# Kernel tuning notes

Measured on AMD Instinct MI355X. Metric: run time of the kernel, lower is better.

Reference implementation:

```python
import jax, jax.numpy as jnp
import numpy as np

L = 10           # outer iterations (module arg L -> sinkhorn n_iter)
N_INNER = 1      # n_inner_iter=1 in SinkhornLoss.forward
EPS = 1.0        # entropic regularization epsilon


def setup_inputs() -> dict:
    key = jax.random.key(0)
    kx, ky = jax.random.split(key)
    x = jax.random.normal(kx, (8192, 32), dtype=jnp.float32)
    y = jax.random.normal(ky, (8192, 32), dtype=jnp.float32)
    return {"x": x, "y": y}


def _sinkhorn_loss(x, y):
    n, m = x.shape[0], y.shape[0]
    # sqeuclidean cdist: [n, m]
    C = (x * x).sum(1)[:, None] + (y * y).sum(1)[None, :] - 2.0 * (x @ y.T)
    # uniform marginals mu = 1/n, nu = 1/m (mu=None, nu=None in source)
    logmu = -jnp.log(jnp.asarray(n, C.dtype))
    lognu = -jnp.log(jnp.asarray(m, C.dtype))
    f0 = jnp.zeros((n,), C.dtype)
    g0 = jnp.zeros((m,), C.dtype)

    def body(carry, _):
        f, g = carry
        # log-domain Sinkhorn updates (stable logsumexp form)
        f = EPS * (logmu - jax.nn.logsumexp((g[None, :] - C) / EPS, axis=1))
        g = EPS * (lognu - jax.nn.logsumexp((f[:, None] - C) / EPS, axis=0))
        return (f, g), None

    (f, g), _ = jax.lax.scan(body, (f0, g0), None, length=L * N_INNER)
    gamma = jnp.exp((f[:, None] + g[None, :] - C) / EPS)  # transport plan [n, m]
    return jnp.sum(C * gamma)  # min_cost = <C, gamma>


def reference(x, y):
    return _sinkhorn_loss(x, y)
```

## Files before the change

### kernel.cpp

```cpp
#include <hip/hip_runtime.h>
#include <math.h>


#define KDIM 32
#define NPS 32
#define NSL_LOSS 16
#define LOG2E 1.44269504088896340736f
#define LN2 0.69314718055994530942f

typedef short short8 __attribute__((ext_vector_type(8)));
typedef float f32x4 __attribute__((ext_vector_type(4)));

__device__ __forceinline__ unsigned short f2bf(float f) {
    unsigned int u = __float_as_uint(f);
    u += 0x7FFF + ((u >> 16) & 1);
    return (unsigned short)(u >> 16);
}
__device__ __forceinline__ float bf2f(unsigned short b) {
    return __uint_as_float(((unsigned int)b) << 16);
}

static __device__ __forceinline__ f32x4 mfma3(const short8 aHt, const short8 aLt,
                                              const short8 bhu, const short8 blu) {
    f32x4 z = {0.f, 0.f, 0.f, 0.f};
    __builtin_amdgcn_s_setprio(1);
    z = __builtin_amdgcn_mfma_f32_16x16x32_bf16(aHt, bhu, z, 0, 0, 0);
    z = __builtin_amdgcn_mfma_f32_16x16x32_bf16(aHt, blu, z, 0, 0, 0);
    z = __builtin_amdgcn_mfma_f32_16x16x32_bf16(aLt, bhu, z, 0, 0, 0);
    __builtin_amdgcn_s_setprio(0);
    return z;
}

__global__ void prep_split(const float* __restrict__ x, const float* __restrict__ y,
                           int nelem,
                           unsigned short* __restrict__ xh, unsigned short* __restrict__ xl,
                           unsigned short* __restrict__ yh, unsigned short* __restrict__ yl) {
    int i4 = (blockIdx.x * 256 + threadIdx.x) * 4;
    if (i4 >= 2 * nelem) return;
    const float* src; unsigned short* dh; unsigned short* dl; int off; float sc;
    if (i4 < nelem) { src = x; dh = xh; dl = xl; off = i4; sc = 2.0f * LOG2E; }
    else            { src = y; dh = yh; dl = yl; off = i4 - nelem; sc = 1.0f; }
    float4 v = *(const float4*)(src + off);
    v.x *= sc; v.y *= sc; v.z *= sc; v.w *= sc;
    ushort4 h, l;
    h.x = f2bf(v.x); l.x = f2bf(v.x - bf2f(h.x));
    h.y = f2bf(v.y); l.y = f2bf(v.y - bf2f(h.y));
    h.z = f2bf(v.z); l.z = f2bf(v.z - bf2f(h.z));
    h.w = f2bf(v.w); l.w = f2bf(v.w - bf2f(h.w));
    *(ushort4*)(dh + off) = h;
    *(ushort4*)(dl + off) = l;
}

__global__ void prep_sq(const float* __restrict__ x, const float* __restrict__ y,
                        int n, float* __restrict__ xsq, float* __restrict__ ysq,
                        float* __restrict__ pb0) {
    int i = blockIdx.x * blockDim.x + threadIdx.x;
    if (i >= 2 * n) return;
    const float* src = (i < n) ? x : y;
    int r = (i < n) ? i : i - n;
    const float4* p = (const float4*)(src + (size_t)r * KDIM);
    float s = 0.f;
#pragma unroll
    for (int q = 0; q < 8; ++q) {
        float4 v = p[q];
        s += v.x * v.x + v.y * v.y + v.z * v.z + v.w * v.w;
    }
    if (i < n) xsq[r] = s;
    else { ysq[r] = s; pb0[r] = __builtin_amdgcn_exp2f(-LOG2E * s); }
}

__global__ __launch_bounds__(256, 4) void sink_pass(
    const unsigned short* __restrict__ Ah, const unsigned short* __restrict__ Alo,
    const unsigned short* __restrict__ Bh, const unsigned short* __restrict__ Blo,
    const float* __restrict__ pb_direct,
    const float* __restrict__ psum_in,
    float* __restrict__ psum_out, int n, float inv_n) {
    __shared__ float pbl[256];
    __shared__ float red[4][64][17];

    const int tid = threadIdx.x;
    const int w = tid >> 6, lane = tid & 63;
    const int mrow = lane & 15, quad = lane >> 4, koff = quad * 8;
    const int i0 = (blockIdx.x * 4 + w) * 64;
    const int jbeg = blockIdx.y * (n / NPS);

    {
        int c = jbeg + tid;
        float b;
        if (pb_direct) {
            b = pb_direct[c];
        } else {
            float s = 0.f;
#pragma unroll
            for (int k = 0; k < NPS; ++k) s += psum_in[(size_t)k * n + c];
            b = inv_n / s;
        }
        pbl[tid] = b;
    }

    short8 aH[4], aL[4];
#pragma unroll
    for (int t = 0; t < 4; ++t) {
        size_t rb = (size_t)(i0 + t * 16 + mrow) * KDIM + koff;
        aH[t] = *(const short8*)(Ah + rb);
        aL[t] = *(const short8*)(Alo + rb);
    }
    __syncthreads();

    float rs[16];
#pragma unroll
    for (int q = 0; q < 16; ++q) rs[q] = 0.f;

    auto ldB = [&](int jt, short8* bh, short8* bl, float* pb) {
        const int j0 = jbeg + jt * 32;
#pragma unroll
        for (int u = 0; u < 2; ++u) {
            size_t rb = (size_t)(j0 + u * 16 + mrow) * KDIM + koff;
            bh[u] = *(const short8*)(Bh + rb);
            bl[u] = *(const short8*)(Blo + rb);
            pb[u] = pbl[jt * 32 + u * 16 + mrow];
        }
    };
    auto eproc = [&](const f32x4 z, int t, float pbu) {
#pragma unroll
        for (int r = 0; r < 4; ++r)
            rs[t * 4 + r] = fmaf(__builtin_amdgcn_exp2f(z[r]), pbu, rs[t * 4 + r]);
    };
    auto compute = [&](short8* bh, short8* bl, float* pb) {
        f32x4 za, zb;
        za = mfma3(aH[0], aL[0], bh[0], bl[0]);
        zb = mfma3(aH[0], aL[0], bh[1], bl[1]);
        eproc(za, 0, pb[0]);
        za = mfma3(aH[1], aL[1], bh[0], bl[0]);
        eproc(zb, 0, pb[1]);
        zb = mfma3(aH[1], aL[1], bh[1], bl[1]);
        eproc(za, 1, pb[0]);
        za = mfma3(aH[2], aL[2], bh[0], bl[0]);
        eproc(zb, 1, pb[1]);
        zb = mfma3(aH[2], aL[2], bh[1], bl[1]);
        eproc(za, 2, pb[0]);
        za = mfma3(aH[3], aL[3], bh[0], bl[0]);
        eproc(zb, 2, pb[1]);
        zb = mfma3(aH[3], aL[3], bh[1], bl[1]);
        eproc(za, 3, pb[0]);
        eproc(zb, 3, pb[1]);
    };

    const int JT = (n / NPS) / 32;
    short8 bh0[2], bl0[2], bh1[2], bl1[2];
    float pb0v[2], pb1v[2];
    ldB(0, bh0, bl0, pb0v);
    for (int jt = 0; jt < JT; jt += 2) {
        ldB(jt + 1, bh1, bl1, pb1v);
        compute(bh0, bl0, pb0v);
        if (jt + 2 < JT) ldB(jt + 2, bh0, bl0, pb0v);
        compute(bh1, bl1, pb1v);
    }

#pragma unroll
    for (int t = 0; t < 4; ++t)
#pragma unroll
        for (int r = 0; r < 4; ++r)
            red[w][t * 16 + quad * 4 + r][mrow] = rs[t * 4 + r];
    __syncthreads();
    {
        int w2 = tid >> 6, row = tid & 63;
        float s = 0.f;
#pragma unroll
        for (int c = 0; c < 16; ++c) s += red[w2][row][c];
        psum_out[(size_t)blockIdx.y * n + (blockIdx.x * 4 + w2) * 64 + row] = s;
    }
}

__global__ __launch_bounds__(256, 4) void sink_loss(
    const unsigned short* __restrict__ Xh, const unsigned short* __restrict__ Xl,
    const unsigned short* __restrict__ Yh, const unsigned short* __restrict__ Yl,
    const float* __restrict__ apsum, const float* __restrict__ bpsum,
    const float* __restrict__ xsq, const float* __restrict__ ysq,
    float* __restrict__ partials, int n, float inv_n) {
    __shared__ float pbL[512];
    __shared__ float ysl[512];
    __shared__ float pal[128];
    __shared__ float xsl[128];
    __shared__ float red[256];

    const int tid = threadIdx.x;
    const int w = tid >> 6, lane = tid & 63;
    const int mrow = lane & 15, quad = lane >> 4, koff = quad * 8;
    const int i0 = (blockIdx.x * 4 + w) * 32;
    const int jbeg = blockIdx.y * (n / NSL_LOSS);

#pragma unroll
    for (int h = 0; h < 2; ++h) {
        int c = tid + h * 256;
        int j = jbeg + c;
        float s = 0.f;
#pragma unroll
        for (int k = 0; k < NPS; ++k) s += bpsum[(size_t)k * n + j];
        pbL[c] = inv_n / s;
        ysl[c] = ysq[j];
    }
    if (tid < 128) {
        int i = blockIdx.x * 128 + tid;
        float s = 0.f;
#pragma unroll
        for (int k = 0; k < NPS; ++k) s += apsum[(size_t)k * n + i];
        pal[tid] = inv_n / s;
        xsl[tid] = xsq[i];
    }

    short8 aH[2], aL[2];
#pragma unroll
    for (int t = 0; t < 2; ++t) {
        size_t rb = (size_t)(i0 + t * 16 + mrow) * KDIM + koff;
        aH[t] = *(const short8*)(Xh + rb);
        aL[t] = *(const short8*)(Xl + rb);
    }
    __syncthreads();

    float pa[8], xs[8];
#pragma unroll
    for (int t = 0; t < 2; ++t)
#pragma unroll
        for (int r = 0; r < 4; ++r) {
            int rl = w * 32 + t * 16 + quad * 4 + r;
            pa[t * 4 + r] = pal[rl];
            xs[t * 4 + r] = xsl[rl];
        }

    float acc = 0.f;

    auto ldB = [&](int jt, short8* bh, short8* bl, float* pb, float* ysv) {
#pragma unroll
        for (int u = 0; u < 2; ++u) {
            int cl = jt * 32 + u * 16 + mrow;
            size_t rb = (size_t)(jbeg + cl) * KDIM + koff;
            bh[u] = *(const short8*)(Yh + rb);
            bl[u] = *(const short8*)(Yl + rb);
            pb[u] = pbL[cl];
            ysv[u] = ysl[cl];
        }
    };
    auto eprocL = [&](const f32x4 z, int t, float pbu, float ysu) {
#pragma unroll
        for (int r = 0; r < 4; ++r) {
            float dd = z[r];
            float e = __builtin_amdgcn_exp2f(dd) * (pa[t * 4 + r] * pbu);
            float cst = fmaf(dd, -LN2, xs[t * 4 + r] + ysu);
            acc = fmaf(cst, e, acc);
        }
    };
    auto compute = [&](short8* bh, short8* bl, float* pb, float* ysv) {
        f32x4 za, zb;
        za = mfma3(aH[0], aL[0], bh[0], bl[0]);
        zb = mfma3(aH[0], aL[0], bh[1], bl[1]);
        eprocL(za, 0, pb[0], ysv[0]);
        za = mfma3(aH[1], aL[1], bh[0], bl[0]);
        eprocL(zb, 0, pb[1], ysv[1]);
        zb = mfma3(aH[1], aL[1], bh[1], bl[1]);
        eprocL(za, 1, pb[0], ysv[0]);
        eprocL(zb, 1, pb[1], ysv[1]);
    };

    const int JT = (n / NSL_LOSS) / 32;
    short8 bh0[2], bl0[2], bh1[2], bl1[2];
    float pb0v[2], pb1v[2], ys0v[2], ys1v[2];
    ldB(0, bh0, bl0, pb0v, ys0v);
    for (int jt = 0; jt < JT; jt += 2) {
        ldB(jt + 1, bh1, bl1, pb1v, ys1v);
        compute(bh0, bl0, pb0v, ys0v);
        if (jt + 2 < JT) ldB(jt + 2, bh0, bl0, pb0v, ys0v);
        compute(bh1, bl1, pb1v, ys1v);
    }

    red[tid] = acc;
    __syncthreads();
#pragma unroll
    for (int s = 128; s > 0; s >>= 1) {
        if (tid < s) red[tid] += red[tid + s];
        __syncthreads();
    }
    if (tid == 0) partials[blockIdx.y * gridDim.x + blockIdx.x] = red[0];
}

__global__ void sink_reduce(const float* __restrict__ p, int nb,
                            float* __restrict__ out) {
    __shared__ float red[256];
    int tid = threadIdx.x;
    float v = 0.f;
    for (int i = tid; i < nb; i += 256) v += p[i];
    red[tid] = v;
    __syncthreads();
#pragma unroll
    for (int s = 128; s > 0; s >>= 1) {
        if (tid < s) red[tid] += red[tid + s];
        __syncthreads();
    }
    if (tid == 0) out[0] = red[0];
}

extern "C" void kernel_launch(void* const* d_in, const int* in_sizes, int n_in,
                              void* d_out, int out_size, void* d_ws, size_t ws_size,
                              hipStream_t stream) {
    const float* x = (const float*)d_in[0];
    const float* y = (const float*)d_in[1];
    const int n = in_sizes[0] / KDIM;
    const int nelem = n * KDIM;
    const float inv_n = 1.0f / (float)n;

    float* ws = (float*)d_ws;
    float* xsq   = ws;
    float* ysq   = ws + n;
    float* pb0   = ws + 2 * n;
    float* apsum = ws + 3 * n;
    float* bpsum = ws + (3 + NPS) * n;
    float* part  = ws + (3 + 2 * NPS) * n;
    unsigned short* us = (unsigned short*)(ws + (4 + 2 * NPS) * n);
    unsigned short* xh = us;
    unsigned short* xl = us + nelem;
    unsigned short* yh = us + 2 * nelem;
    unsigned short* yl = us + 3 * nelem;

    dim3 pgrid(n / 256, NPS);
    dim3 lgrid(n / 128, NSL_LOSS);

    prep_split<<<(2 * nelem / 4 + 255) / 256, 256, 0, stream>>>(x, y, nelem, xh, xl, yh, yl);
    prep_sq<<<(2 * n + 255) / 256, 256, 0, stream>>>(x, y, n, xsq, ysq, pb0);

    sink_pass<<<pgrid, 256, 0, stream>>>(xh, xl, yh, yl, pb0, nullptr, apsum, n, inv_n);
    sink_pass<<<pgrid, 256, 0, stream>>>(yh, yl, xh, xl, nullptr, apsum, bpsum, n, inv_n);
    for (int t = 1; t < 10; ++t) {
        sink_pass<<<pgrid, 256, 0, stream>>>(xh, xl, yh, yl, nullptr, bpsum, apsum, n, inv_n);
        sink_pass<<<pgrid, 256, 0, stream>>>(yh, yl, xh, xl, nullptr, apsum, bpsum, n, inv_n);
    }
    sink_loss<<<lgrid, 256, 0, stream>>>(xh, xl, yh, yl, apsum, bpsum, xsq, ysq, part, n, inv_n);
    sink_reduce<<<1, 256, 0, stream>>>(part, (n / 128) * NSL_LOSS, (float*)d_out);
}
```

Measured before the change: 399.2 us.

## Stage B tiles through swizzled shared memory with double buffering in sink_pass

Each block now loads its B high/low bf16 tiles cooperatively into a double-buffered, XOR-swizzled LDS buffer, and waves read them from LDS. Previously each of the four waves fetched the same B rows from global memory on its own. This cuts redundant global and L2 traffic, at the cost of a __syncthreads per 32-column tile and extra LDS use. The occupancy hint is also raised from 4 to 5 blocks per CU.

```diff
diff --git a/kernel.cpp b/kernel.cpp
--- a/kernel.cpp
+++ b/kernel.cpp
@@ -69,7 +69,7 @@
     else { ysq[r] = s; pb0[r] = __builtin_amdgcn_exp2f(-LOG2E * s); }
 }
 
-__global__ __launch_bounds__(256, 4) void sink_pass(
+__global__ __launch_bounds__(256, 5) void sink_pass(
     const unsigned short* __restrict__ Ah, const unsigned short* __restrict__ Alo,
     const unsigned short* __restrict__ Bh, const unsigned short* __restrict__ Blo,
     const float* __restrict__ pb_direct,
@@ -77,6 +77,7 @@
     float* __restrict__ psum_out, int n, float inv_n) {
     __shared__ float pbl[256];
     __shared__ float red[4][64][17];
+    __shared__ unsigned short Bs[2][2][32 * KDIM];
 
     const int tid = threadIdx.x;
     const int w = tid >> 6, lane = tid & 63;
@@ -105,20 +106,39 @@
         aH[t] = *(const short8*)(Ah + rb);
         aL[t] = *(const short8*)(Alo + rb);
     }
+
+    const int s_reg = w >> 1;
+    const int s_col = (w & 1) * 16 + (lane >> 2);
+    const int s_slot = lane & 3;
+    const int s_swz = s_slot ^ ((s_col >> 1) & 3);
+    const unsigned short* s_base = (s_reg == 0 ? Bh : Blo);
+    unsigned short* s_dst = &Bs[0][0][0] + (size_t)0;
+
+    auto stage_src = [&](int jt) {
+        return s_base + (size_t)(jbeg + jt * 32 + s_col) * KDIM + s_slot * 8;
+    };
+    auto stage_write = [&](int b, short8 v) {
+        *(short8*)&Bs[b][s_reg][s_col * KDIM + s_swz * 8] = v;
+    };
+
+    {
+        short8 v0 = *(const short8*)stage_src(0);
+        stage_write(0, v0);
+    }
     __syncthreads();
 
     float rs[16];
 #pragma unroll
     for (int q = 0; q < 16; ++q) rs[q] = 0.f;
 
-    auto ldB = [&](int jt, short8* bh, short8* bl, float* pb) {
-        const int j0 = jbeg + jt * 32;
+    auto ldB = [&](int b, int jt, short8* bh, short8* bl, float* pb) {
 #pragma unroll
         for (int u = 0; u < 2; ++u) {
-            size_t rb = (size_t)(j0 + u * 16 + mrow) * KDIM + koff;
-            bh[u] = *(const short8*)(Bh + rb);
-            bl[u] = *(const short8*)(Blo + rb);
-            pb[u] = pbl[jt * 32 + u * 16 + mrow];
+            int cl = u * 16 + mrow;
+            int sl = quad ^ ((cl >> 1) & 3);
+            bh[u] = *(const short8*)&Bs[b][0][cl * KDIM + sl * 8];
+            bl[u] = *(const short8*)&Bs[b][1][cl * KDIM + sl * 8];
+            pb[u] = pbl[jt * 32 + cl];
         }
     };
     auto eproc = [&](const f32x4 z, int t, float pbu) {
@@ -147,14 +167,16 @@
     };
 
     const int JT = (n / NPS) / 32;
-    short8 bh0[2], bl0[2], bh1[2], bl1[2];
-    float pb0v[2], pb1v[2];
-    ldB(0, bh0, bl0, pb0v);
-    for (int jt = 0; jt < JT; jt += 2) {
-        ldB(jt + 1, bh1, bl1, pb1v);
-        compute(bh0, bl0, pb0v);
-        if (jt + 2 < JT) ldB(jt + 2, bh0, bl0, pb0v);
-        compute(bh1, bl1, pb1v);
+    short8 bh[2], bl[2];
+    float pbv[2];
+    for (int jt = 0; jt < JT; ++jt) {
+        const int b = jt & 1;
+        short8 v;
+        if (jt + 1 < JT) v = *(const short8*)stage_src(jt + 1);
+        ldB(b, jt, bh, bl, pbv);
+        compute(bh, bl, pbv);
+        if (jt + 1 < JT) stage_write(b ^ 1, v);
+        __syncthreads();
     }
 
 #pragma unroll
```

After: 543.0 us. 36.0% more time.
